# Performance work log

Measured on AMD Instinct MI355X. Metric: run time of the kernel, lower is better.

Reference implementation:

```python
import jax, jax.numpy as jnp
import numpy as np

N, E, D_IN, HID, H = 50000, 800000, 128, 64, 2
C = HID  # per-head dim (out_channels)


def _lin_params(key, fan_in, fan_out):
    kw, kb = jax.random.split(key)
    s = 1.0 / np.sqrt(fan_in)
    W = jax.random.uniform(kw, (fan_in, fan_out), jnp.float32, -s, s)
    b = jax.random.uniform(kb, (fan_out,), jnp.float32, -s, s)
    return W, b


def setup_inputs() -> dict:
    key = jax.random.key(0)
    ks = jax.random.split(key, 14)
    x = jax.random.normal(ks[0], (N, D_IN), jnp.float32)
    edge_index = jax.random.randint(ks[1], (2, E), 0, N, jnp.int32)
    inp = {"x": x, "edge_index": edge_index}
    dims = [D_IN, HID, HID]
    i = 2
    for L, d_in in enumerate(dims, start=1):
        for nm, fo in (("q", H * C), ("k", H * C), ("v", H * C), ("s", HID)):
            W, b = _lin_params(ks[i], d_in, fo)
            inp[f"W{L}{nm}"] = W
            inp[f"b{L}{nm}"] = b
            i += 1
            if i >= 14:
                ks = jax.random.split(ks[-1], 14)
                i = 0
    return inp


def _transformer_conv(x, src, dst, Wq, bq, Wk, bk, Wv, bv, Ws, bs):
    # x: [N, d_in] -> out: [N, HID]
    q = (x @ Wq + bq).reshape(N, H, C)
    k = (x @ Wk + bk).reshape(N, H, C)
    v = (x @ Wv + bv).reshape(N, H, C)
    qi = q[dst]                      # [E, H, C] gather at destination (query)
    kj = k[src]                      # [E, H, C] gather at source (key)
    alpha = jnp.sum(qi * kj, axis=-1) / jnp.sqrt(jnp.float32(C))  # [E, H]
    amax = jax.ops.segment_max(alpha, dst, num_segments=N)        # [N, H]
    ex = jnp.exp(alpha - amax[dst])                               # [E, H]
    denom = jax.ops.segment_sum(ex, dst, num_segments=N)          # [N, H]
    attn = ex / (denom[dst] + 1e-16)                              # [E, H]
    msg = v[src] * attn[:, :, None]                               # [E, H, C]
    out = jax.ops.segment_sum(msg, dst, num_segments=N)           # [N, H, C]
    out = out.mean(axis=1)                                        # concat=False: head mean
    return out + x @ Ws + bs                                      # root skip


def reference(x, edge_index,
              W1q, b1q, W1k, b1k, W1v, b1v, W1s, b1s,
              W2q, b2q, W2k, b2k, W2v, b2v, W2s, b2s,
              W3q, b3q, W3k, b3k, W3v, b3v, W3s, b3s):
    src, dst = edge_index[0], edge_index[1]
    h = jax.nn.relu(_transformer_conv(x, src, dst, W1q, b1q, W1k, b1k, W1v, b1v, W1s, b1s))
    h = jax.nn.relu(_transformer_conv(h, src, dst, W2q, b2q, W2k, b2k, W2v, b2v, W2s, b2s))
    h = jax.nn.relu(_transformer_conv(h, src, dst, W3q, b3q, W3k, b3k, W3v, b3v, W3s, b3s))
    return h
```

## Files before the change

### kernel.cpp

```cpp
#include <hip/hip_runtime.h>
#include <cstdint>

typedef _Float16 f16;
typedef __attribute__((ext_vector_type(2))) _Float16 f16x2;
typedef __attribute__((ext_vector_type(4))) _Float16 f16x4;
typedef __attribute__((ext_vector_type(8))) _Float16 f16x8;
typedef __attribute__((ext_vector_type(4))) float f32x4;

#if defined(__has_builtin)
# if __has_builtin(__builtin_amdgcn_fdot2)
#  define HAVE_FDOT2 1
# endif
#endif


__global__ void hist_kernel(const int* __restrict__ dst, int* __restrict__ cnt, int E) {
    int e = blockIdx.x * blockDim.x + threadIdx.x;
    if (e < E) atomicAdd(&cnt[dst[e]], 1);
}

__global__ __launch_bounds__(256) void block_scan_kernel(
    const int* __restrict__ cnt, int* __restrict__ rowptr,
    int* __restrict__ partials, int n) {
    __shared__ int lds[256];
    int tid = threadIdx.x;
    int i = blockIdx.x * 256 + tid;
    int v = (i < n) ? cnt[i] : 0;
    lds[tid] = v;
    __syncthreads();
    for (int off = 1; off < 256; off <<= 1) {
        int t = (tid >= off) ? lds[tid - off] : 0;
        __syncthreads();
        lds[tid] += t;
        __syncthreads();
    }
    if (i < n) rowptr[i + 1] = lds[tid];
    if (tid == 255) partials[blockIdx.x] = lds[255];
}

__global__ __launch_bounds__(256) void partial_scan_kernel(int* __restrict__ partials, int nb) {
    __shared__ int lds[256];
    int tid = threadIdx.x;
    int v = (tid < nb) ? partials[tid] : 0;
    lds[tid] = v;
    __syncthreads();
    for (int off = 1; off < 256; off <<= 1) {
        int t = (tid >= off) ? lds[tid - off] : 0;
        __syncthreads();
        lds[tid] += t;
        __syncthreads();
    }
    if (tid < nb) partials[tid] = lds[tid] - v;
}

__global__ __launch_bounds__(256) void add_offsets_kernel(
    int* __restrict__ rowptr, const int* __restrict__ partials, int n) {
    int i = blockIdx.x * 256 + threadIdx.x;
    if (i < n) rowptr[i + 1] += partials[blockIdx.x];
    if (i == 0) rowptr[0] = 0;
}

__global__ void scatter_kernel(const int* __restrict__ src, const int* __restrict__ dst,
                               const int* __restrict__ rowptr, int* __restrict__ cnt,
                               int* __restrict__ src_sorted, int E) {
    int e = blockIdx.x * blockDim.x + threadIdx.x;
    if (e < E) {
        int d = dst[e];
        int p = rowptr[d] + atomicAdd(&cnt[d], 1);
        src_sorted[p] = src[e];
    }
}


__global__ __launch_bounds__(256) void prep_w_kernel(
    const float* __restrict__ Wq, const float* __restrict__ Wk,
    const float* __restrict__ Wv, const float* __restrict__ Ws,
    const float* __restrict__ bq, const float* __restrict__ bk,
    const float* __restrict__ bv, const float* __restrict__ bs,
    f16* __restrict__ Wt, float* __restrict__ bias, int K) {
    int idx = blockIdx.x * 256 + threadIdx.x;
    if (idx < 448) {
        bias[idx] = (idx < 128) ? bq[idx]
                  : (idx < 256) ? bk[idx - 128]
                  : (idx < 384) ? bv[idx - 256]
                  : bs[idx - 384];
    }
    if (idx >= 448 * K) return;
    int c = idx / K, k = idx - c * K;
    float v;
    if (c < 128)      v = Wq[k * 128 + c];
    else if (c < 256) v = Wk[k * 128 + (c - 128)];
    else if (c < 384) v = Wv[k * 128 + (c - 256)];
    else              v = Ws[k * 64 + (c - 384)];
    Wt[(size_t)c * K + k] = (f16)v;
}


template <int K, bool F32IN>
__global__ __launch_bounds__(256) void gemm_qkvs_kernel(
    const void* __restrict__ Xv, const f16* __restrict__ Wt,
    const float* __restrict__ bias, f16* __restrict__ out, int M) {
    __shared__ f16 xa[64 * K];
    __shared__ f16 wb[64 * K];
    int row0 = blockIdx.x * 64;
    int tid = threadIdx.x;

    if (F32IN) {
        const float* X = (const float*)Xv;
        constexpr int CPR = K / 4;
        for (int c = tid; c < 64 * CPR; c += 256) {
            int r = c / CPR, kc = c % CPR;
            int gr = row0 + r;
            float4 v = {0.f, 0.f, 0.f, 0.f};
            if (gr < M) v = *(const float4*)(X + (size_t)gr * K + kc * 4);
            f16x4 hv = {(f16)v.x, (f16)v.y, (f16)v.z, (f16)v.w};
            int off = (r * K + kc * 4) * 2;
            off ^= (r & 7) << 4;
            *(f16x4*)((char*)xa + off) = hv;
        }
    } else {
        const f16* X = (const f16*)Xv;
        constexpr int CPR = K / 8;
        for (int c = tid; c < 64 * CPR; c += 256) {
            int r = c / CPR, kc = c % CPR;
            int gr = row0 + r;
            uint4 v = {0, 0, 0, 0};
            if (gr < M) v = *(const uint4*)(X + (size_t)gr * K + kc * 8);
            int off = (r * K + kc * 8) * 2;
            off ^= (r & 7) << 4;
            *(uint4*)((char*)xa + off) = v;
        }
    }
    __syncthreads();

    int lane = tid & 63, wid = tid >> 6;
    int fr = lane & 15, fk = lane >> 4;
    int arow = wid * 16 + fr;
    constexpr int NK = K / 32;
    f16x8 af[NK];
    #pragma unroll
    for (int ks = 0; ks < NK; ++ks) {
        int aoff = (arow * K + ks * 32 + fk * 8) * 2;
        aoff ^= (arow & 7) << 4;
        af[ks] = *(f16x8*)((char*)xa + aoff);
    }

    int orow = row0 + wid * 16 + fk * 4;
    constexpr int CPRW = K / 8;
    for (int ct = 0; ct < 7; ++ct) {
        if (ct > 0) __syncthreads();
        int col0 = ct * 64;
        for (int c = tid; c < 64 * CPRW; c += 256) {
            int r = c / CPRW, kc = c % CPRW;
            uint4 v = *(const uint4*)(Wt + (size_t)(col0 + r) * K + kc * 8);
            int off = (r * K + kc * 8) * 2;
            off ^= (r & 7) << 4;
            *(uint4*)((char*)wb + off) = v;
        }
        __syncthreads();

        f32x4 acc[4] = {};
        #pragma unroll
        for (int ks = 0; ks < NK; ++ks) {
            #pragma unroll
            for (int cf = 0; cf < 4; ++cf) {
                int brow = cf * 16 + fr;
                int boff = (brow * K + ks * 32 + fk * 8) * 2;
                boff ^= (brow & 7) << 4;
                f16x8 bf = *(f16x8*)((char*)wb + boff);
                acc[cf] = __builtin_amdgcn_mfma_f32_16x16x32_f16(af[ks], bf, acc[cf], 0, 0, 0);
            }
        }

        int ocol = col0 + fr;
        #pragma unroll
        for (int cf = 0; cf < 4; ++cf) {
            float b = bias[ocol + cf * 16];
            #pragma unroll
            for (int r = 0; r < 4; ++r) {
                int gr = orow + r;
                if (gr < M) out[(size_t)gr * 448 + ocol + cf * 16] = (f16)(acc[cf][r] + b);
            }
        }
    }
}


__global__ __launch_bounds__(256) void attn_kernel(
    const f16* __restrict__ T,
    const int* __restrict__ rowptr, const int* __restrict__ srcs,
    f16* __restrict__ hout, float* __restrict__ fout, int n, int final_layer) {
    int node = blockIdx.x * 4 + (threadIdx.x >> 6);
    if (node >= n) return;
    int lane = threadIdx.x & 63;
    int c8 = lane & 7, e2 = lane >> 4;
    const size_t base = (size_t)node * 448;
    const int coff = ((lane >> 3) & 1) * 64 + c8 * 8;

    f16x8 q = *(const f16x8*)(T + base + coff);
    float m = -__builtin_inff(), s = 0.f;
    float av[8] = {};

    int beg = rowptr[node], end = rowptr[node + 1];
    for (int i0 = beg; i0 < end; i0 += 4) {
        int i = i0 + e2;
        bool valid = (i < end);
        int sidx = srcs[valid ? i : (end - 1)];
        const f16* p = T + (size_t)sidx * 448 + coff;
        f16x8 kv = *(const f16x8*)(p + 128);
        f16x8 vv = *(const f16x8*)(p + 256);
        float d = 0.f;
#ifdef HAVE_FDOT2
        #pragma unroll
        for (int j = 0; j < 4; ++j) {
            f16x2 qq = {q[2 * j], q[2 * j + 1]};
            f16x2 kk = {kv[2 * j], kv[2 * j + 1]};
            d = __builtin_amdgcn_fdot2(qq, kk, d, false);
        }
#else
        #pragma unroll
        for (int j = 0; j < 8; ++j) d += (float)q[j] * (float)kv[j];
#endif
        d += __shfl_xor(d, 1);
        d += __shfl_xor(d, 2);
        d += __shfl_xor(d, 4);
        d *= 0.125f;
        if (!valid) d = -__builtin_inff();

        if (__any(d > m + 6.f)) {
            float dmax = fmaxf(d, __shfl_xor(d, 16));
            dmax = fmaxf(dmax, __shfl_xor(dmax, 32));
            float nm = fmaxf(m, dmax);
            float f = __expf(m - nm);
            s *= f;
            #pragma unroll
            for (int j = 0; j < 8; ++j) av[j] *= f;
            m = nm;
        }
        float pe = __expf(d - m);
        s += pe;
        #pragma unroll
        for (int j = 0; j < 8; ++j) av[j] += pe * (float)vv[j];
    }

    s += __shfl_xor(s, 16);
    s += __shfl_xor(s, 32);
    float inv = 1.0f / (s + 1e-16f);
    float r[8];
    #pragma unroll
    for (int j = 0; j < 8; ++j) {
        float a = av[j];
        a += __shfl_xor(a, 16);
        a += __shfl_xor(a, 32);
        r[j] = a * inv;
    }
    #pragma unroll
    for (int j = 0; j < 8; ++j) r[j] = 0.5f * (r[j] + __shfl_xor(r[j], 8));

    if (lane < 8) {
        f16x8 sk = *(const f16x8*)(T + base + 384 + c8 * 8);
        #pragma unroll
        for (int j = 0; j < 8; ++j) r[j] = fmaxf(r[j] + (float)sk[j], 0.f);
        if (final_layer) {
            float4* dst4 = (float4*)(fout + (size_t)node * 64 + c8 * 8);
            dst4[0] = make_float4(r[0], r[1], r[2], r[3]);
            dst4[1] = make_float4(r[4], r[5], r[6], r[7]);
        } else {
            f16x8 o = {(f16)r[0], (f16)r[1], (f16)r[2], (f16)r[3],
                       (f16)r[4], (f16)r[5], (f16)r[6], (f16)r[7]};
            *(f16x8*)(hout + (size_t)node * 64 + c8 * 8) = o;
        }
    }
}


extern "C" void kernel_launch(void* const* d_in, const int* in_sizes, int n_in,
                              void* d_out, int out_size, void* d_ws, size_t ws_size,
                              hipStream_t stream) {
    const float* x = (const float*)d_in[0];
    const int* ei  = (const int*)d_in[1];
    const int N = in_sizes[0] / 128;
    const int E = in_sizes[1] / 2;
    const int* src = ei;
    const int* dst = ei + E;

    const float* Wq[3] = {(const float*)d_in[2],  (const float*)d_in[10], (const float*)d_in[18]};
    const float* bq[3] = {(const float*)d_in[3],  (const float*)d_in[11], (const float*)d_in[19]};
    const float* Wk[3] = {(const float*)d_in[4],  (const float*)d_in[12], (const float*)d_in[20]};
    const float* bk[3] = {(const float*)d_in[5],  (const float*)d_in[13], (const float*)d_in[21]};
    const float* Wv[3] = {(const float*)d_in[6],  (const float*)d_in[14], (const float*)d_in[22]};
    const float* bv[3] = {(const float*)d_in[7],  (const float*)d_in[15], (const float*)d_in[23]};
    const float* Wsk[3]= {(const float*)d_in[8],  (const float*)d_in[16], (const float*)d_in[24]};
    const float* bsk[3]= {(const float*)d_in[9],  (const float*)d_in[17], (const float*)d_in[25]};

    char* p = (char*)d_ws;
    int* rowptr   = (int*)p; p += (size_t)(N + 1) * 4;
    int* cnt      = (int*)p; p += (size_t)N * 4;
    int* srcs     = (int*)p; p += (size_t)E * 4;
    int* partials = (int*)p; p += 256 * 4;
    p = (char*)(((uintptr_t)p + 255) & ~(uintptr_t)255);
    f16* Xh   = (f16*)p; p += (size_t)N * 64 * 2;
    f16* QKVS = (f16*)p; p += (size_t)N * 448 * 2;
    f16* Wt   = (f16*)p; p += (size_t)448 * 128 * 2;
    float* bias = (float*)p; p += 448 * 4;
    if ((size_t)(p - (char*)d_ws) > ws_size) return;

    int nb = (N + 255) / 256;
    hipMemsetAsync(cnt, 0, (size_t)N * 4, stream);
    hist_kernel<<<(E + 255) / 256, 256, 0, stream>>>(dst, cnt, E);
    block_scan_kernel<<<nb, 256, 0, stream>>>(cnt, rowptr, partials, N);
    partial_scan_kernel<<<1, 256, 0, stream>>>(partials, nb);
    add_offsets_kernel<<<nb, 256, 0, stream>>>(rowptr, partials, N);
    hipMemsetAsync(cnt, 0, (size_t)N * 4, stream);
    scatter_kernel<<<(E + 255) / 256, 256, 0, stream>>>(src, dst, rowptr, cnt, srcs, E);

    int gx = (N + 63) / 64;
    for (int l = 0; l < 3; ++l) {
        int K = (l == 0) ? 128 : 64;
        prep_w_kernel<<<(448 * K + 255) / 256, 256, 0, stream>>>(
            Wq[l], Wk[l], Wv[l], Wsk[l], bq[l], bk[l], bv[l], bsk[l], Wt, bias, K);
        if (l == 0)
            gemm_qkvs_kernel<128, true><<<gx, 256, 0, stream>>>(x, Wt, bias, QKVS, N);
        else
            gemm_qkvs_kernel<64, false><<<gx, 256, 0, stream>>>(Xh, Wt, bias, QKVS, N);
        attn_kernel<<<(N + 3) / 4, 256, 0, stream>>>(
            QKVS, rowptr, srcs, Xh, (float*)d_out, N, (l == 2) ? 1 : 0);
    }
}
```

Measured before the change: 373.6 us.

## Restructure attention to 8 edges per iteration, double-buffer GEMM weight tiles

The attention kernel now has each lane group handle both heads for one edge, so eight edges are processed per iteration instead of four. The next source index is prefetched one iteration ahead to hide the dependent index load. The QKVS GEMM double-buffers its weight tiles in LDS so the next tile loads while the current one runs through MFMA, dropping one barrier per tile at the cost of doubled LDS. Weight prep for all three layers is hoisted into separate buffers launched up front, removing serialization between layers.

New measurement: 380.3 us. No clear change (+1.8%).

```diff
diff --git a/kernel.cpp b/kernel.cpp
--- a/kernel.cpp
+++ b/kernel.cpp
@@ -101,9 +101,10 @@
     const void* __restrict__ Xv, const f16* __restrict__ Wt,
     const float* __restrict__ bias, f16* __restrict__ out, int M) {
     __shared__ f16 xa[64 * K];
-    __shared__ f16 wb[64 * K];
+    __shared__ f16 wb[2][64 * K];
     int row0 = blockIdx.x * 64;
     int tid = threadIdx.x;
+    constexpr int CPRW = K / 8;
 
     if (F32IN) {
         const float* X = (const float*)Xv;
@@ -120,9 +121,8 @@
         }
     } else {
         const f16* X = (const f16*)Xv;
-        constexpr int CPR = K / 8;
-        for (int c = tid; c < 64 * CPR; c += 256) {
-            int r = c / CPR, kc = c % CPR;
+        for (int c = tid; c < 64 * CPRW; c += 256) {
+            int r = c / CPRW, kc = c % CPRW;
             int gr = row0 + r;
             uint4 v = {0, 0, 0, 0};
             if (gr < M) v = *(const uint4*)(X + (size_t)gr * K + kc * 8);
@@ -130,6 +130,13 @@
             off ^= (r & 7) << 4;
             *(uint4*)((char*)xa + off) = v;
         }
+    }
+    for (int c = tid; c < 64 * CPRW; c += 256) {
+        int r = c / CPRW, kc = c % CPRW;
+        uint4 v = *(const uint4*)(Wt + (size_t)r * K + kc * 8);
+        int off = (r * K + kc * 8) * 2;
+        off ^= (r & 7) << 4;
+        *(uint4*)((char*)wb[0] + off) = v;
     }
     __syncthreads();
 
@@ -146,19 +153,20 @@
     }
 
     int orow = row0 + wid * 16 + fk * 4;
-    constexpr int CPRW = K / 8;
     for (int ct = 0; ct < 7; ++ct) {
-        if (ct > 0) __syncthreads();
-        int col0 = ct * 64;
-        for (int c = tid; c < 64 * CPRW; c += 256) {
-            int r = c / CPRW, kc = c % CPRW;
-            uint4 v = *(const uint4*)(Wt + (size_t)(col0 + r) * K + kc * 8);
-            int off = (r * K + kc * 8) * 2;
-            off ^= (r & 7) << 4;
-            *(uint4*)((char*)wb + off) = v;
-        }
-        __syncthreads();
-
+        if (ct < 6) {
+            int col0 = (ct + 1) * 64;
+            f16* dstb = wb[(ct + 1) & 1];
+            for (int c = tid; c < 64 * CPRW; c += 256) {
+                int r = c / CPRW, kc = c % CPRW;
+                uint4 v = *(const uint4*)(Wt + (size_t)(col0 + r) * K + kc * 8);
+                int off = (r * K + kc * 8) * 2;
+                off ^= (r & 7) << 4;
+                *(uint4*)((char*)dstb + off) = v;
+            }
+        }
+
+        const f16* curb = wb[ct & 1];
         f32x4 acc[4] = {};
         #pragma unroll
         for (int ks = 0; ks < NK; ++ks) {
@@ -167,12 +175,12 @@
                 int brow = cf * 16 + fr;
                 int boff = (brow * K + ks * 32 + fk * 8) * 2;
                 boff ^= (brow & 7) << 4;
-                f16x8 bf = *(f16x8*)((char*)wb + boff);
+                f16x8 bf = *(f16x8*)((char*)curb + boff);
                 acc[cf] = __builtin_amdgcn_mfma_f32_16x16x32_f16(af[ks], bf, acc[cf], 0, 0, 0);
             }
         }
 
-        int ocol = col0 + fr;
+        int ocol = ct * 64 + fr;
         #pragma unroll
         for (int cf = 0; cf < 4; ++cf) {
             float b = bias[ocol + cf * 16];
@@ -182,6 +190,7 @@
                 if (gr < M) out[(size_t)gr * 448 + ocol + cf * 16] = (f16)(acc[cf][r] + b);
             }
         }
+        __syncthreads();
     }
 }
 
@@ -193,82 +202,104 @@
     int node = blockIdx.x * 4 + (threadIdx.x >> 6);
     if (node >= n) return;
     int lane = threadIdx.x & 63;
-    int c8 = lane & 7, e2 = lane >> 4;
+    int c8 = lane & 7, eg = lane >> 3;
     const size_t base = (size_t)node * 448;
-    const int coff = ((lane >> 3) & 1) * 64 + c8 * 8;
-
-    f16x8 q = *(const f16x8*)(T + base + coff);
-    float m = -__builtin_inff(), s = 0.f;
-    float av[8] = {};
+    const int co = c8 * 8;
+
+    f16x8 q0 = *(const f16x8*)(T + base + co);
+    f16x8 q1 = *(const f16x8*)(T + base + 64 + co);
+    float m0 = -__builtin_inff(), m1 = -__builtin_inff();
+    float s0 = 0.f, s1 = 0.f;
+    float av0[8] = {}, av1[8] = {};
 
     int beg = rowptr[node], end = rowptr[node + 1];
-    for (int i0 = beg; i0 < end; i0 += 4) {
-        int i = i0 + e2;
-        bool valid = (i < end);
-        int sidx = srcs[valid ? i : (end - 1)];
-        const f16* p = T + (size_t)sidx * 448 + coff;
-        f16x8 kv = *(const f16x8*)(p + 128);
-        f16x8 vv = *(const f16x8*)(p + 256);
-        float d = 0.f;
+    if (beg < end) {
+        int nsrc = srcs[min(beg + eg, end - 1)];
+        for (int i0 = beg; i0 < end; i0 += 8) {
+            int i = i0 + eg;
+            bool valid = (i < end);
+            int sidx = nsrc;
+            if (i0 + 8 < end) nsrc = srcs[min(i + 8, end - 1)];
+
+            const f16* p = T + (size_t)sidx * 448 + co;
+            f16x8 k0 = *(const f16x8*)(p + 128);
+            f16x8 k1 = *(const f16x8*)(p + 192);
+            f16x8 v0 = *(const f16x8*)(p + 256);
+            f16x8 v1 = *(const f16x8*)(p + 320);
+
+            float d0 = 0.f, d1 = 0.f;
 #ifdef HAVE_FDOT2
-        #pragma unroll
-        for (int j = 0; j < 4; ++j) {
-            f16x2 qq = {q[2 * j], q[2 * j + 1]};
-            f16x2 kk = {kv[2 * j], kv[2 * j + 1]};
-            d = __builtin_amdgcn_fdot2(qq, kk, d, false);
-        }
+            #pragma unroll
+            for (int j = 0; j < 4; ++j) {
+                f16x2 a0 = {q0[2 * j], q0[2 * j + 1]};
+                f16x2 b0 = {k0[2 * j], k0[2 * j + 1]};
+                d0 = __builtin_amdgcn_fdot2(a0, b0, d0, false);
+                f16x2 a1 = {q1[2 * j], q1[2 * j + 1]};
+                f16x2 b1 = {k1[2 * j], k1[2 * j + 1]};
+                d1 = __builtin_amdgcn_fdot2(a1, b1, d1, false);
+            }
 #else
-        #pragma unroll
-        for (int j = 0; j < 8; ++j) d += (float)q[j] * (float)kv[j];
+            #pragma unroll
+            for (int j = 0; j < 8; ++j) {
+                d0 += (float)q0[j] * (float)k0[j];
+                d1 += (float)q1[j] * (float)k1[j];
+            }
 #endif
-        d += __shfl_xor(d, 1);
-        d += __shfl_xor(d, 2);
-        d += __shfl_xor(d, 4);
-        d *= 0.125f;
-        if (!valid) d = -__builtin_inff();
-
-        if (__any(d > m + 6.f)) {
-            float dmax = fmaxf(d, __shfl_xor(d, 16));
-            dmax = fmaxf(dmax, __shfl_xor(dmax, 32));
-            float nm = fmaxf(m, dmax);
-            float f = __expf(m - nm);
-            s *= f;
-            #pragma unroll
-            for (int j = 0; j < 8; ++j) av[j] *= f;
-            m = nm;
-        }
-        float pe = __expf(d - m);
-        s += pe;
-        #pragma unroll
-        for (int j = 0; j < 8; ++j) av[j] += pe * (float)vv[j];
-    }
-
-    s += __shfl_xor(s, 16);
-    s += __shfl_xor(s, 32);
-    float inv = 1.0f / (s + 1e-16f);
+            d0 += __shfl_xor(d0, 1); d1 += __shfl_xor(d1, 1);
+            d0 += __shfl_xor(d0, 2); d1 += __shfl_xor(d1, 2);
+            d0 += __shfl_xor(d0, 4); d1 += __shfl_xor(d1, 4);
+            d0 *= 0.125f; d1 *= 0.125f;
+            if (!valid) { d0 = -__builtin_inff(); d1 = -__builtin_inff(); }
+
+            if (__any(d0 > m0 + 6.f || d1 > m1 + 6.f)) {
+                float t0 = d0, t1 = d1;
+                t0 = fmaxf(t0, __shfl_xor(t0, 8));  t1 = fmaxf(t1, __shfl_xor(t1, 8));
+                t0 = fmaxf(t0, __shfl_xor(t0, 16)); t1 = fmaxf(t1, __shfl_xor(t1, 16));
+                t0 = fmaxf(t0, __shfl_xor(t0, 32)); t1 = fmaxf(t1, __shfl_xor(t1, 32));
+                float nm0 = fmaxf(m0, t0), nm1 = fmaxf(m1, t1);
+                float f0 = __expf(m0 - nm0), f1 = __expf(m1 - nm1);
+                s0 *= f0; s1 *= f1;
+                #pragma unroll
+                for (int j = 0; j < 8; ++j) { av0[j] *= f0; av1[j] *= f1; }
+                m0 = nm0; m1 = nm1;
+            }
+            float p0 = __expf(d0 - m0);
+            float p1 = __expf(d1 - m1);
+            s0 += p0; s1 += p1;
+            #pragma unroll
+            for (int j = 0; j < 8; ++j) {
+                av0[j] += p0 * (float)v0[j];
+                av1[j] += p1 * (float)v1[j];
+            }
+        }
+    }
+
+    s0 += __shfl_xor(s0, 8);  s1 += __shfl_xor(s1, 8);
+    s0 += __shfl_xor(s0, 16); s1 += __shfl_xor(s1, 16);
+    s0 += __shfl_xor(s0, 32); s1 += __shfl_xor(s1, 32);
+    float inv0 = 1.0f / (s0 + 1e-16f), inv1 = 1.0f / (s1 + 1e-16f);
     float r[8];
     #pragma unroll
     for (int j = 0; j < 8; ++j) {
-        float a = av[j];
-        a += __shfl_xor(a, 16);
-        a += __shfl_xor(a, 32);
-        r[j] = a * inv;
-    }
-    #pragma unroll
-    for (int j = 0; j < 8; ++j) r[j] = 0.5f * (r[j] + __shfl_xor(r[j], 8));
+        float a0 = av0[j], a1 = av1[j];
+        a0 += __shfl_xor(a0, 8);  a1 += __shfl_xor(a1, 8);
+        a0 += __shfl_xor(a0, 16); a1 += __shfl_xor(a1, 16);
+        a0 += __shfl_xor(a0, 32); a1 += __shfl_xor(a1, 32);
+        r[j] = 0.5f * (a0 * inv0 + a1 * inv1);
+    }
 
     if (lane < 8) {
-        f16x8 sk = *(const f16x8*)(T + base + 384 + c8 * 8);
+        f16x8 sk = *(const f16x8*)(T + base + 384 + co);
         #pragma unroll
         for (int j = 0; j < 8; ++j) r[j] = fmaxf(r[j] + (float)sk[j], 0.f);
         if (final_layer) {
-            float4* dst4 = (float4*)(fout + (size_t)node * 64 + c8 * 8);
+            float4* dst4 = (float4*)(fout + (size_t)node * 64 + co);
             dst4[0] = make_float4(r[0], r[1], r[2], r[3]);
             dst4[1] = make_float4(r[4], r[5], r[6], r[7]);
         } else {
             f16x8 o = {(f16)r[0], (f16)r[1], (f16)r[2], (f16)r[3],
                        (f16)r[4], (f16)r[5], (f16)r[6], (f16)r[7]};
-            *(f16x8*)(hout + (size_t)node * 64 + c8 * 8) = o;
+            *(f16x8*)(hout + (size_t)node * 64 + co) = o;
         }
     }
 }
@@ -301,9 +332,22 @@
     p = (char*)(((uintptr_t)p + 255) & ~(uintptr_t)255);
     f16* Xh   = (f16*)p; p += (size_t)N * 64 * 2;
     f16* QKVS = (f16*)p; p += (size_t)N * 448 * 2;
-    f16* Wt   = (f16*)p; p += (size_t)448 * 128 * 2;
-    float* bias = (float*)p; p += 448 * 4;
+    f16* Wt0  = (f16*)p; p += (size_t)448 * 128 * 2;
+    f16* Wt1  = (f16*)p; p += (size_t)448 * 64 * 2;
+    f16* Wt2  = (f16*)p; p += (size_t)448 * 64 * 2;
+    float* bias0 = (float*)p; p += 448 * 4;
+    float* bias1 = (float*)p; p += 448 * 4;
+    float* bias2 = (float*)p; p += 448 * 4;
     if ((size_t)(p - (char*)d_ws) > ws_size) return;
+
+    f16* Wt[3] = {Wt0, Wt1, Wt2};
+    float* bias[3] = {bias0, bias1, bias2};
+
+    for (int l = 0; l < 3; ++l) {
+        int K = (l == 0) ? 128 : 64;
+        prep_w_kernel<<<(448 * K + 255) / 256, 256, 0, stream>>>(
+            Wq[l], Wk[l], Wv[l], Wsk[l], bq[l], bk[l], bv[l], bsk[l], Wt[l], bias[l], K);
+    }
 
     int nb = (N + 255) / 256;
     hipMemsetAsync(cnt, 0, (size_t)N * 4, stream);
@@ -316,13 +360,10 @@
 
     int gx = (N + 63) / 64;
     for (int l = 0; l < 3; ++l) {
-        int K = (l == 0) ? 128 : 64;
-        prep_w_kernel<<<(448 * K + 255) / 256, 256, 0, stream>>>(
-            Wq[l], Wk[l], Wv[l], Wsk[l], bq[l], bk[l], bv[l], bsk[l], Wt, bias, K);
         if (l == 0)
-            gemm_qkvs_kernel<128, true><<<gx, 256, 0, stream>>>(x, Wt, bias, QKVS, N);
+            gemm_qkvs_kernel<128, true><<<gx, 256, 0, stream>>>(x, Wt[l], bias[l], QKVS, N);
         else
-            gemm_qkvs_kernel<64, false><<<gx, 256, 0, stream>>>(Xh, Wt, bias, QKVS, N);
+            gemm_qkvs_kernel<64, false><<<gx, 256, 0, stream>>>(Xh, Wt[l], bias[l], QKVS, N);
         attn_kernel<<<(N + 3) / 4, 256, 0, stream>>>(
             QKVS, rowptr, srcs, Xh, (float*)d_out, N, (l == 2) ? 1 : 0);
     }
```
